# Kernel optimization log

Hardware: AMD Instinct MI355X
Metric: run time of the kernel (lower is better)

The kernel has to match this reference:

```python
import jax, jax.numpy as jnp
import numpy as np


def setup_inputs() -> dict:
    key = jax.random.key(0)
    k1, k2, k3 = jax.random.split(key, 3)
    B, T, C = 4, 2048, 1024
    dim = C
    x = jax.random.normal(k1, (B, T, C), dtype=jnp.float32)
    # torch nn.Linear weight layout: [out_features, in_features], scaled like kaiming-uniform-ish
    w_qkv = jax.random.normal(k2, (3 * dim, dim), dtype=jnp.float32) * (1.0 / np.sqrt(dim))
    w_out = jax.random.normal(k3, (dim, dim), dtype=jnp.float32) * (1.0 / np.sqrt(dim))
    return {"x": x, "w_qkv": w_qkv, "w_out": w_out}


def reference(x, w_qkv, w_out):
    B, T, C = x.shape
    n_heads = 16
    head_dim = C // n_heads

    qkv = jnp.einsum("btc,dc->btd", x, w_qkv)  # [B,T,3C]
    q, k, v = jnp.split(qkv, 3, axis=-1)

    def split_heads(t):
        return t.reshape(B, T, n_heads, head_dim).transpose(0, 2, 1, 3)  # [B,H,T,hd]

    q, k, v = split_heads(q), split_heads(k), split_heads(v)

    scale = 1.0 / np.sqrt(head_dim).astype(np.float32)
    scores = jnp.einsum("bhqd,bhkd->bhqk", q, k) * scale  # [B,H,T,T]
    causal = jnp.tril(jnp.ones((T, T), dtype=bool))
    scores = jnp.where(causal, scores, jnp.finfo(scores.dtype).min)
    attn = jax.nn.softmax(scores, axis=-1)
    out = jnp.einsum("bhqk,bhkd->bhqd", attn, v)  # [B,H,T,hd]
    out = out.transpose(0, 2, 1, 3).reshape(B, T, C)
    return jnp.einsum("btc,dc->btd", out, w_out)
```

## Files before the change

### kernel.cpp

```cpp
#include <hip/hip_runtime.h>
#include <hip/hip_bf16.h>


typedef __attribute__((ext_vector_type(8))) short bf16x8;
typedef __attribute__((ext_vector_type(4))) float f32x4;
typedef __attribute__((ext_vector_type(16))) float f32x16;
typedef __attribute__((ext_vector_type(2))) unsigned uint2v;

#define GLOBAL_AS __attribute__((address_space(1)))
#define LDS_AS __attribute__((address_space(3)))

__device__ __forceinline__ unsigned short f2b_rne(float f) {
  unsigned u = __float_as_uint(f);
  unsigned r = u + 0x7fffu + ((u >> 16) & 1u);
  return (unsigned short)(r >> 16);
}

__device__ __forceinline__ unsigned cvt_pk_bf16(float lo, float hi) {
  unsigned r;
  asm("v_cvt_pk_bf16_f32 %0, %1, %2" : "=v"(r) : "v"(lo), "v"(hi));
  return r;
}

__device__ __forceinline__ void gload_lds16(const void* g, void* l) {
  __builtin_amdgcn_global_load_lds((const GLOBAL_AS void*)g, (LDS_AS void*)l, 16, 0, 0);
}

__global__ void f32_to_bf16_vec(const float* __restrict__ src,
                                unsigned short* __restrict__ dst, int n4) {
  int i = blockIdx.x * blockDim.x + threadIdx.x;
  int stride = gridDim.x * blockDim.x;
  for (; i < n4; i += stride) {
    float4 v = reinterpret_cast<const float4*>(src)[i];
    ushort4 o;
    o.x = f2b_rne(v.x); o.y = f2b_rne(v.y);
    o.z = f2b_rne(v.z); o.w = f2b_rne(v.w);
    reinterpret_cast<ushort4*>(dst)[i] = o;
  }
}

__global__ __launch_bounds__(256)
void v_transpose(const unsigned short* __restrict__ qkv,
                 unsigned short* __restrict__ vt) {
  __shared__ __align__(16) unsigned short Ts[64][64];
  const int tc = blockIdx.x, bh = blockIdx.y;
  const int b = bh >> 4, hed = bh & 15;
  const int t0 = tc * 64;
  const int tid = threadIdx.x;
  {
    const int r = tid >> 2, cb = (tid & 3) * 2;
    const unsigned short* src =
        qkv + (size_t)(b * 2048 + t0 + r) * 3072 + 2048 + hed * 64;
    bf16x8 v0 = *(const bf16x8*)(src + cb * 8);
    bf16x8 v1 = *(const bf16x8*)(src + cb * 8 + 8);
    *(bf16x8*)&Ts[r][(cb ^ (r & 7)) * 8] = v0;
    *(bf16x8*)&Ts[r][((cb + 1) ^ (r & 7)) * 8] = v1;
  }
  __syncthreads();
  const int d = tid >> 2;
  unsigned short* dst = vt + ((size_t)bh * 64 + d) * 2048 + t0;
#pragma unroll
  for (int tb2 = 0; tb2 < 2; ++tb2) {
    int tb = (tid & 3) * 2 + tb2;
    union { unsigned short s[8]; bf16x8 v; } o;
#pragma unroll
    for (int i = 0; i < 8; ++i) {
      int row = tb * 8 + i;
      o.s[i] = Ts[row][(((d >> 3) ^ (row & 7)) * 8) + (d & 7)];
    }
    *(bf16x8*)(dst + tb * 8) = o.v;
  }
}

__global__ __launch_bounds__(512, 2)
void gemm_qkv(const unsigned short* __restrict__ A,
              const unsigned short* __restrict__ B,
              unsigned short* __restrict__ C) {
  const int K = 1024, N = 3072;
  __shared__ __align__(16) unsigned short As[2][2][128 * 64];
  __shared__ __align__(16) unsigned short Bs[2][128 * 64];

  const int tid = threadIdx.x, wid = tid >> 6, lane = tid & 63;
  const int l31 = lane & 31, h = lane >> 5;
  const int wgid = ((int)blockIdx.x & 7) * 96 + ((int)blockIdx.x >> 3);
  const int bx = wgid % 24, by = wgid / 24;
  const int m0 = by * 256, n0 = bx * 128;
  const int wr = wid >> 1, wc = wid & 1;

  auto stage = [&](int t, int buf) {
    const int k0 = t * 64;
    const int r8 = lane >> 3;
    const int blk = (lane & 7) ^ r8;
#pragma unroll
    for (int hh = 0; hh < 2; ++hh)
#pragma unroll
      for (int r = 0; r < 2; ++r) {
        int row = r * 64 + wid * 8 + r8;
        gload_lds16(A + (size_t)(m0 + hh * 128 + row) * K + k0 + blk * 8,
                    &As[buf][hh][r * 4096 + wid * 512]);
      }
#pragma unroll
    for (int r = 0; r < 2; ++r) {
      int row = r * 64 + wid * 8 + r8;
      gload_lds16(B + (size_t)(n0 + row) * K + k0 + blk * 8,
                  &Bs[buf][r * 4096 + wid * 512]);
    }
  };

  f32x16 acc[2][2] = {};

  stage(0, 0);
  asm volatile("s_waitcnt vmcnt(0)" ::: "memory");
  __builtin_amdgcn_sched_barrier(0);
  __builtin_amdgcn_s_barrier();
  __builtin_amdgcn_sched_barrier(0);

  int cur = 0;
  for (int t = 0; t < 16; ++t) {
    if (t + 1 < 16) stage(t + 1, cur ^ 1);

    bf16x8 af[2][4], bfr[2][4];
#pragma unroll
    for (int mi = 0; mi < 2; ++mi) {
      int row = (wr & 1) * 64 + mi * 32 + l31;
#pragma unroll
      for (int ks = 0; ks < 4; ++ks) {
        int chunk = (ks * 2 + h) ^ (row & 7);
        af[mi][ks] = *(const bf16x8*)&As[cur][wr >> 1][row * 64 + chunk * 8];
      }
    }
#pragma unroll
    for (int ni = 0; ni < 2; ++ni) {
      int row = wc * 64 + ni * 32 + l31;
#pragma unroll
      for (int ks = 0; ks < 4; ++ks) {
        int chunk = (ks * 2 + h) ^ (row & 7);
        bfr[ni][ks] = *(const bf16x8*)&Bs[cur][row * 64 + chunk * 8];
      }
    }
    __builtin_amdgcn_s_setprio(1);
#pragma unroll
    for (int ks = 0; ks < 4; ++ks)
#pragma unroll
      for (int mi = 0; mi < 2; ++mi)
#pragma unroll
        for (int ni = 0; ni < 2; ++ni)
          acc[mi][ni] = __builtin_amdgcn_mfma_f32_32x32x16_bf16(
              af[mi][ks], bfr[ni][ks], acc[mi][ni], 0, 0, 0);
    __builtin_amdgcn_s_setprio(0);

    asm volatile("s_waitcnt vmcnt(0)" ::: "memory");
    __builtin_amdgcn_sched_barrier(0);
    __builtin_amdgcn_s_barrier();
    __builtin_amdgcn_sched_barrier(0);
    cur ^= 1;
  }

#pragma unroll
  for (int mi = 0; mi < 2; ++mi)
#pragma unroll
    for (int ni = 0; ni < 2; ++ni)
#pragma unroll
      for (int reg = 0; reg < 16; ++reg) {
        int row = m0 + wr * 64 + mi * 32 + (reg & 3) + 8 * (reg >> 2) + 4 * h;
        int col = n0 + wc * 64 + ni * 32 + l31;
        C[(size_t)row * N + col] = f2b_rne(acc[mi][ni][reg]);
      }
}

__global__ __launch_bounds__(256)
void gemm_nt(const unsigned short* __restrict__ A,
             const unsigned short* __restrict__ B,
             float* __restrict__ Cout, int M, int N, int K) {
  __shared__ __align__(16) unsigned short As[128][32];
  __shared__ __align__(16) unsigned short Bs[128][32];
  const int tid = threadIdx.x;
  const int w = tid >> 6, lane = tid & 63;
  const int l16 = lane & 15, lg = lane >> 4;
  const int wrow = (w >> 1) * 64, wcol = (w & 1) * 64;
  const int m0 = blockIdx.y * 128, n0 = blockIdx.x * 128;

  f32x4 acc[4][4] = {};

  auto stage = [&](int k0) {
#pragma unroll
    for (int c2 = 0; c2 < 2; ++c2) {
      int c = 2 * w + c2;
      const unsigned short* ga =
          A + (size_t)(m0 + 16 * c + (lane >> 2)) * K + k0 + (lane & 3) * 8;
      gload_lds16(ga, &As[16 * c][0]);
      const unsigned short* gb =
          B + (size_t)(n0 + 16 * c + (lane >> 2)) * K + k0 + (lane & 3) * 8;
      gload_lds16(gb, &Bs[16 * c][0]);
    }
  };

  stage(0);
  __syncthreads();
  const int nk = K >> 5;
  for (int ks = 0; ks < nk; ++ks) {
    bf16x8 af[4], bfr[4];
#pragma unroll
    for (int mi = 0; mi < 4; ++mi)
      af[mi] = *(const bf16x8*)&As[wrow + mi * 16 + l16][lg * 8];
#pragma unroll
    for (int ni = 0; ni < 4; ++ni)
      bfr[ni] = *(const bf16x8*)&Bs[wcol + ni * 16 + l16][lg * 8];
    __syncthreads();
    if (ks + 1 < nk) stage((ks + 1) * 32);
#pragma unroll
    for (int mi = 0; mi < 4; ++mi)
#pragma unroll
      for (int ni = 0; ni < 4; ++ni)
        acc[mi][ni] = __builtin_amdgcn_mfma_f32_16x16x32_bf16(
            af[mi], bfr[ni], acc[mi][ni], 0, 0, 0);
    __syncthreads();
  }

#pragma unroll
  for (int mi = 0; mi < 4; ++mi)
#pragma unroll
    for (int ni = 0; ni < 4; ++ni)
#pragma unroll
      for (int j = 0; j < 4; ++j) {
        int row = m0 + wrow + mi * 16 + lg * 4 + j;
        int col = n0 + wcol + ni * 16 + l16;
        Cout[(size_t)row * N + col] = acc[mi][ni][j];
      }
}

__global__ __launch_bounds__(256, 2)
void attn_fwd(const unsigned short* __restrict__ qkv,
              const unsigned short* __restrict__ vt,
              unsigned short* __restrict__ out) {
  const int T = 2048, C3 = 3072;
  __shared__ __align__(16) unsigned short Ks[2][64][64];
  __shared__ __align__(16) unsigned short Vs[2][64][64];
  __shared__ float Bc[4][32];

  const int tid = threadIdx.x, w = tid >> 6, lane = tid & 63;
  const int l31 = lane & 31, h = lane >> 5;
  const int wgid = (blockIdx.x & 7) * 64 + (blockIdx.x >> 3);
  const int local = wgid & 63, xcd = wgid >> 6;
  const int qidx = local >> 3, bhl = local & 7;
  const int bh = xcd * 8 + bhl;
  const int qt = (qidx < 4) ? (7 - qidx) : (qidx - 4);
  const int b = bh >> 4, hed = bh & 15;
  const int qw = qt * 256 + w * 64;
  const size_t rowbase = (size_t)b * T * C3;
  const int hoff = hed * 64;
  const unsigned short* vbase = vt + (size_t)bh * 64 * 2048;
  const float c2 = 0.18033688f;

  auto stageK = [&](int kv0, int buf) {
#pragma unroll
    for (int pp = 0; pp < 2; ++pp) {
      int chunk = w * 2 + pp;
      int row = chunk * 8 + (lane >> 3);
      int blk = (lane & 7) ^ (lane >> 3);
      gload_lds16(
          qkv + rowbase + (size_t)(kv0 + row) * C3 + 1024 + hoff + blk * 8,
          &Ks[buf][chunk * 8][0]);
    }
  };
  auto stageV = [&](int kv0, int buf) {
#pragma unroll
    for (int pp = 0; pp < 2; ++pp) {
      int chunk = w * 2 + pp;
      int drow = chunk * 8 + (lane >> 3);
      int blk = (lane & 7) ^ (lane >> 3);
      gload_lds16(vbase + (size_t)drow * 2048 + kv0 + blk * 8,
                  &Vs[buf][chunk * 8][0]);
    }
  };

  bf16x8 qf0[4], qf1[4];
  {
    const unsigned short* qp0 =
        qkv + rowbase + (size_t)(qw + l31) * C3 + hoff + h * 8;
    const unsigned short* qp1 = qp0 + 32 * C3;
#pragma unroll
    for (int s = 0; s < 4; ++s) {
      qf0[s] = *(const bf16x8*)(qp0 + 16 * s);
      qf1[s] = *(const bf16x8*)(qp1 + 16 * s);
    }
  }

  f32x16 oacc0[2] = {}, oacc1[2] = {};
  float mr0 = -1e30f, mr1 = -1e30f, sum0 = 0.f, sum1 = 0.f;

  stageK(0, 0);
  stageV(0, 0);

  auto do_half = [&](f32x16 (&sacc)[2], int qx, float& mr, float& sm,
                     f32x16 (&oc)[2], int t, int kv0, int cur) {
    if (kv0 + 64 > qx) {
      int q_abs = qx + l31;
#pragma unroll
      for (int kt = 0; kt < 2; ++kt)
#pragma unroll
        for (int r = 0; r < 16; ++r) {
          int kv_abs = kv0 + kt * 32 + (r & 3) + 8 * (r >> 2) + 4 * h;
          if (kv_abs > q_abs) sacc[kt][r] = -1e30f;
        }
    }
    float mx[8];
#pragma unroll
    for (int g = 0; g < 8; ++g)
      mx[g] = fmaxf(fmaxf(sacc[g >> 2][(g & 3) * 4 + 0],
                          sacc[g >> 2][(g & 3) * 4 + 1]),
                    fmaxf(sacc[g >> 2][(g & 3) * 4 + 2],
                          sacc[g >> 2][(g & 3) * 4 + 3]));
    float tm = fmaxf(fmaxf(fmaxf(mx[0], mx[1]), fmaxf(mx[2], mx[3])),
                     fmaxf(fmaxf(mx[4], mx[5]), fmaxf(mx[6], mx[7])));
    tm = fmaxf(tm, __shfl_xor(tm, 32));
    if (t == 0) {
      mr = tm;
    } else if (!__all(tm <= mr + 16.0f)) {
      float mnew = fmaxf(mr, tm);
      float corr = __builtin_amdgcn_exp2f((mr - mnew) * c2);
      sm *= corr;
      if (h == 0) Bc[w][l31] = corr;
      mr = mnew;
      asm volatile("s_waitcnt lgkmcnt(0)" ::: "memory");
#pragma unroll
      for (int r = 0; r < 16; ++r) {
        float cr = Bc[w][(r & 3) + 8 * (r >> 2) + 4 * h];
        oc[0][r] *= cr;
        oc[1][r] *= cr;
      }
    }
    float m2 = mr * c2;
    float s0 = 0.f, s1 = 0.f, s2 = 0.f, s3 = 0.f;
#pragma unroll
    for (int kt = 0; kt < 2; ++kt)
#pragma unroll
      for (int r = 0; r < 16; r += 4) {
        float p0 = __builtin_amdgcn_exp2f(fmaf(sacc[kt][r + 0], c2, -m2));
        float p1 = __builtin_amdgcn_exp2f(fmaf(sacc[kt][r + 1], c2, -m2));
        float p2 = __builtin_amdgcn_exp2f(fmaf(sacc[kt][r + 2], c2, -m2));
        float p3 = __builtin_amdgcn_exp2f(fmaf(sacc[kt][r + 3], c2, -m2));
        sacc[kt][r + 0] = p0; sacc[kt][r + 1] = p1;
        sacc[kt][r + 2] = p2; sacc[kt][r + 3] = p3;
        s0 += p0; s1 += p1; s2 += p2; s3 += p3;
      }
    float sl = (s0 + s1) + (s2 + s3);
    sm += sl + __shfl_xor(sl, 32);
    unsigned pk[16];
#pragma unroll
    for (int kt = 0; kt < 2; ++kt)
#pragma unroll
      for (int r = 0; r < 16; r += 2)
        pk[kt * 8 + (r >> 1)] = cvt_pk_bf16(sacc[kt][r], sacc[kt][r + 1]);
    __builtin_amdgcn_s_setprio(1);
#pragma unroll
    for (int sg = 0; sg < 4; ++sg) {
      const int kt = sg >> 1, s = sg & 1;
      const int base = kt * 8 + 4 * s;
      uint2v r02 = __builtin_amdgcn_permlane32_swap(pk[base], pk[base + 2],
                                                    false, false);
      uint2v r13 = __builtin_amdgcn_permlane32_swap(pk[base + 1], pk[base + 3],
                                                    false, false);
      union { unsigned u[4]; bf16x8 v; } Afr;
      Afr.u[0] = r02.x; Afr.u[1] = r13.x;
      Afr.u[2] = r02.y; Afr.u[3] = r13.y;
#pragma unroll
      for (int dt = 0; dt < 2; ++dt) {
        int d = dt * 32 + l31;
        int blk = (2 * sg + h) ^ (d & 7);
        bf16x8 vf = *(const bf16x8*)&Vs[cur][d][blk * 8];
        oc[dt] = __builtin_amdgcn_mfma_f32_32x32x16_bf16(Afr.v, vf,
                                                         oc[dt], 0, 0, 0);
      }
    }
    __builtin_amdgcn_s_setprio(0);
  };

  int cur = 0;
  const int ntiles = 4 * qt + 4;
  for (int t = 0; t < ntiles; ++t) {
    const int kv0 = t * 64;
    __builtin_amdgcn_s_barrier();
    if (t + 1 < ntiles) {
      stageK(kv0 + 64, cur ^ 1);
      stageV(kv0 + 64, cur ^ 1);
      asm volatile("s_waitcnt vmcnt(4)" ::: "memory");
    } else {
      asm volatile("s_waitcnt vmcnt(0)" ::: "memory");
    }
    __builtin_amdgcn_s_barrier();
    __builtin_amdgcn_sched_barrier(0);

    if (kv0 <= qw) {
      f32x16 sacc0[2] = {}, sacc1[2] = {};
      __builtin_amdgcn_s_setprio(1);
#pragma unroll
      for (int s = 0; s < 4; ++s) {
#pragma unroll
        for (int kt = 0; kt < 2; ++kt) {
          int row = kt * 32 + l31;
          int blk = (2 * s + h) ^ (row & 7);
          bf16x8 kf = *(const bf16x8*)&Ks[cur][row][blk * 8];
          sacc0[kt] = __builtin_amdgcn_mfma_f32_32x32x16_bf16(kf, qf0[s],
                                                              sacc0[kt], 0, 0, 0);
          sacc1[kt] = __builtin_amdgcn_mfma_f32_32x32x16_bf16(kf, qf1[s],
                                                              sacc1[kt], 0, 0, 0);
        }
      }
      __builtin_amdgcn_s_setprio(0);
      do_half(sacc0, qw, mr0, sum0, oacc0, t, kv0, cur);
      do_half(sacc1, qw + 32, mr1, sum1, oacc1, t, kv0, cur);
    }
    cur ^= 1;
  }

#pragma unroll
  for (int X = 0; X < 2; ++X) {
    float sm = X ? sum1 : sum0;
    if (h == 0) Bc[w][l31] = 1.0f / sm;
    asm volatile("s_waitcnt lgkmcnt(0)" ::: "memory");
#pragma unroll
    for (int r = 0; r < 16; ++r) {
      int ql = (r & 3) + 8 * (r >> 2) + 4 * h;
      float inv = Bc[w][ql];
      int q_abs = qw + 32 * X + ql;
#pragma unroll
      for (int dt = 0; dt < 2; ++dt) {
        float v = (X ? oacc1 : oacc0)[dt][r] * inv;
        out[(size_t)(b * T + q_abs) * 1024 + hoff + dt * 32 + l31] =
            f2b_rne(v);
      }
    }
    __builtin_amdgcn_s_barrier();
  }
}

extern "C" void kernel_launch(void* const* d_in, const int* in_sizes, int n_in,
                              void* d_out, int out_size, void* d_ws,
                              size_t ws_size, hipStream_t stream) {
  const float* x = (const float*)d_in[0];
  const float* w_qkv = (const float*)d_in[1];
  const float* w_out = (const float*)d_in[2];
  float* out = (float*)d_out;

  const int M = 8192, C = 1024, C3 = 3072;

  unsigned short* xb = (unsigned short*)d_ws;
  unsigned short* wqkvb = xb + (size_t)M * C;
  unsigned short* woutb = wqkvb + (size_t)C3 * C;
  unsigned short* qkv = woutb + (size_t)C * C;
  unsigned short* vtb = qkv + (size_t)M * C3;
  unsigned short* attno = xb;

  f32_to_bf16_vec<<<1024, 256, 0, stream>>>(x, xb, M * C / 4);
  f32_to_bf16_vec<<<512, 256, 0, stream>>>(w_qkv, wqkvb, C3 * C / 4);
  f32_to_bf16_vec<<<256, 256, 0, stream>>>(w_out, woutb, C * C / 4);

  gemm_qkv<<<768, 512, 0, stream>>>(xb, wqkvb, qkv);

  v_transpose<<<dim3(32, 64), 256, 0, stream>>>(qkv, vtb);

  attn_fwd<<<512, 256, 0, stream>>>(qkv, vtb, attno);

  gemm_nt<<<dim3(C / 128, M / 128), 256, 0, stream>>>(attno, woutb, out,
                                                      M, C, C);
}
```

Measured before the change: 192.2 us.

## Templatize big GEMM, reuse it for output projection, and relax pipeline waits

Turns the QKV GEMM kernel into a template over N and output type, and uses it for the output projection in place of the simpler 128x128 gemm_nt kernel. The main loop now issues the next stage's loads, then waits only until the previous stage's loads have landed (vmcnt(6)) instead of draining all loads after the compute. The min-waves-per-EU hint is dropped from the launch bounds. The output projection then runs on 256 large 256x128 tiles, fewer workgroups than there are compute units, which may underfill the GPU.

```diff
diff --git a/kernel.cpp b/kernel.cpp
--- a/kernel.cpp
+++ b/kernel.cpp
@@ -72,18 +72,21 @@
   }
 }
 
-__global__ __launch_bounds__(512, 2)
-void gemm_qkv(const unsigned short* __restrict__ A,
+template <int N, int OUT_BF16>
+__global__ __launch_bounds__(512)
+void gemm_big(const unsigned short* __restrict__ A,
               const unsigned short* __restrict__ B,
-              unsigned short* __restrict__ C) {
-  const int K = 1024, N = 3072;
+              void* __restrict__ Cout) {
+  const int K = 1024;
   __shared__ __align__(16) unsigned short As[2][2][128 * 64];
   __shared__ __align__(16) unsigned short Bs[2][128 * 64];
 
   const int tid = threadIdx.x, wid = tid >> 6, lane = tid & 63;
   const int l31 = lane & 31, h = lane >> 5;
-  const int wgid = ((int)blockIdx.x & 7) * 96 + ((int)blockIdx.x >> 3);
-  const int bx = wgid % 24, by = wgid / 24;
+  const int NBX = N / 128;
+  const int nwg8 = (int)gridDim.x >> 3;
+  const int wgid = ((int)blockIdx.x & 7) * nwg8 + ((int)blockIdx.x >> 3);
+  const int bx = wgid % NBX, by = wgid / NBX;
   const int m0 = by * 256, n0 = bx * 128;
   const int wr = wid >> 1, wc = wid & 1;
 
@@ -110,14 +113,18 @@
   f32x16 acc[2][2] = {};
 
   stage(0, 0);
-  asm volatile("s_waitcnt vmcnt(0)" ::: "memory");
-  __builtin_amdgcn_sched_barrier(0);
-  __builtin_amdgcn_s_barrier();
-  __builtin_amdgcn_sched_barrier(0);
 
   int cur = 0;
   for (int t = 0; t < 16; ++t) {
-    if (t + 1 < 16) stage(t + 1, cur ^ 1);
+    __builtin_amdgcn_s_barrier();
+    if (t + 1 < 16) {
+      stage(t + 1, cur ^ 1);
+      asm volatile("s_waitcnt vmcnt(6)" ::: "memory");
+    } else {
+      asm volatile("s_waitcnt vmcnt(0)" ::: "memory");
+    }
+    __builtin_amdgcn_s_barrier();
+    __builtin_amdgcn_sched_barrier(0);
 
     bf16x8 af[2][4], bfr[2][4];
 #pragma unroll
@@ -148,11 +155,6 @@
           acc[mi][ni] = __builtin_amdgcn_mfma_f32_32x32x16_bf16(
               af[mi][ks], bfr[ni][ks], acc[mi][ni], 0, 0, 0);
     __builtin_amdgcn_s_setprio(0);
-
-    asm volatile("s_waitcnt vmcnt(0)" ::: "memory");
-    __builtin_amdgcn_sched_barrier(0);
-    __builtin_amdgcn_s_barrier();
-    __builtin_amdgcn_sched_barrier(0);
     cur ^= 1;
   }
 
@@ -164,68 +166,11 @@
       for (int reg = 0; reg < 16; ++reg) {
         int row = m0 + wr * 64 + mi * 32 + (reg & 3) + 8 * (reg >> 2) + 4 * h;
         int col = n0 + wc * 64 + ni * 32 + l31;
-        C[(size_t)row * N + col] = f2b_rne(acc[mi][ni][reg]);
-      }
-}
-
-__global__ __launch_bounds__(256)
-void gemm_nt(const unsigned short* __restrict__ A,
-             const unsigned short* __restrict__ B,
-             float* __restrict__ Cout, int M, int N, int K) {
-  __shared__ __align__(16) unsigned short As[128][32];
-  __shared__ __align__(16) unsigned short Bs[128][32];
-  const int tid = threadIdx.x;
-  const int w = tid >> 6, lane = tid & 63;
-  const int l16 = lane & 15, lg = lane >> 4;
-  const int wrow = (w >> 1) * 64, wcol = (w & 1) * 64;
-  const int m0 = blockIdx.y * 128, n0 = blockIdx.x * 128;
-
-  f32x4 acc[4][4] = {};
-
-  auto stage = [&](int k0) {
-#pragma unroll
-    for (int c2 = 0; c2 < 2; ++c2) {
-      int c = 2 * w + c2;
-      const unsigned short* ga =
-          A + (size_t)(m0 + 16 * c + (lane >> 2)) * K + k0 + (lane & 3) * 8;
-      gload_lds16(ga, &As[16 * c][0]);
-      const unsigned short* gb =
-          B + (size_t)(n0 + 16 * c + (lane >> 2)) * K + k0 + (lane & 3) * 8;
-      gload_lds16(gb, &Bs[16 * c][0]);
-    }
-  };
-
-  stage(0);
-  __syncthreads();
-  const int nk = K >> 5;
-  for (int ks = 0; ks < nk; ++ks) {
-    bf16x8 af[4], bfr[4];
-#pragma unroll
-    for (int mi = 0; mi < 4; ++mi)
-      af[mi] = *(const bf16x8*)&As[wrow + mi * 16 + l16][lg * 8];
-#pragma unroll
-    for (int ni = 0; ni < 4; ++ni)
-      bfr[ni] = *(const bf16x8*)&Bs[wcol + ni * 16 + l16][lg * 8];
-    __syncthreads();
-    if (ks + 1 < nk) stage((ks + 1) * 32);
-#pragma unroll
-    for (int mi = 0; mi < 4; ++mi)
-#pragma unroll
-      for (int ni = 0; ni < 4; ++ni)
-        acc[mi][ni] = __builtin_amdgcn_mfma_f32_16x16x32_bf16(
-            af[mi], bfr[ni], acc[mi][ni], 0, 0, 0);
-    __syncthreads();
-  }
-
-#pragma unroll
-  for (int mi = 0; mi < 4; ++mi)
-#pragma unroll
-    for (int ni = 0; ni < 4; ++ni)
-#pragma unroll
-      for (int j = 0; j < 4; ++j) {
-        int row = m0 + wrow + mi * 16 + lg * 4 + j;
-        int col = n0 + wcol + ni * 16 + l16;
-        Cout[(size_t)row * N + col] = acc[mi][ni][j];
+        if (OUT_BF16)
+          ((unsigned short*)Cout)[(size_t)row * N + col] =
+              f2b_rne(acc[mi][ni][reg]);
+        else
+          ((float*)Cout)[(size_t)row * N + col] = acc[mi][ni][reg];
       }
 }
 
@@ -456,12 +401,11 @@
   f32_to_bf16_vec<<<512, 256, 0, stream>>>(w_qkv, wqkvb, C3 * C / 4);
   f32_to_bf16_vec<<<256, 256, 0, stream>>>(w_out, woutb, C * C / 4);
 
-  gemm_qkv<<<768, 512, 0, stream>>>(xb, wqkvb, qkv);
+  gemm_big<3072, 1><<<768, 512, 0, stream>>>(xb, wqkvb, qkv);
 
   v_transpose<<<dim3(32, 64), 256, 0, stream>>>(qkv, vtb);
 
   attn_fwd<<<512, 256, 0, stream>>>(qkv, vtb, attno);
 
-  gemm_nt<<<dim3(C / 128, M / 128), 256, 0, stream>>>(attno, woutb, out,
-                                                      M, C, C);
-}
+  gemm_big<1024, 0><<<256, 512, 0, stream>>>(attno, woutb, out);
+}
```

Result: no change. 189.8 us (-1.2%).
